# Optimization experiments

Measured on AMD Instinct MI355X. Metric: run time of the kernel, lower is better.

The kernel has to match this reference:

```python
import jax, jax.numpy as jnp
import numpy as np

U, S, D = 4096, 8192, 32
NUM_REGIONS = 128
GA = 0.1


def setup_inputs() -> dict:
    key = jax.random.key(0)
    k1, k2, k3, k4, k5, k6 = jax.random.split(key, 6)
    user_emb = jax.random.normal(k1, (U, D), dtype=jnp.float32) * 0.01
    item_emb = jax.random.normal(k2, (S, D), dtype=jnp.float32) * 0.01
    train_mask = jax.random.randint(k3, (U, S), 0, 2, dtype=jnp.int32)
    true_qos = jax.random.normal(k4, (U, S), dtype=jnp.float32)
    us_lossweight = jax.random.uniform(k5, (U, S), dtype=jnp.float32)
    region_index = jax.random.randint(k6, (U,), 0, NUM_REGIONS, dtype=jnp.int32)
    return {
        "user_emb": user_emb,
        "item_emb": item_emb,
        "train_mask": train_mask,
        "true_qos": true_qos,
        "us_lossweight": us_lossweight,
        "region_index": region_index,
    }


def _region_loss(user_emb, region_index):
    # per-region sums and counts via a single segment reduction
    sums = jax.ops.segment_sum(user_emb, region_index, num_segments=NUM_REGIONS)  # [R, D]
    counts = jax.ops.segment_sum(jnp.ones((user_emb.shape[0],), dtype=user_emb.dtype),
                                 region_index, num_segments=NUM_REGIONS)  # [R]
    cnt = counts[region_index]                      # [U]
    loo_mean = (sums[region_index] - user_emb) / jnp.maximum(cnt - 1.0, 1.0)[:, None]
    dev = jnp.abs(user_emb - loo_mean)              # [U, D]
    # regions with a single user are skipped in the original loop
    valid = (cnt > 1.0)[:, None]
    return jnp.sum(jnp.where(valid, dev, 0.0))


def reference(user_emb, item_emb, train_mask, true_qos, us_lossweight, region_index):
    pre_qos = (user_emb @ item_emb.T) * train_mask.astype(user_emb.dtype)  # [U, S]
    mse = (pre_qos - true_qos) ** 2
    loss = jnp.sum(us_lossweight * mse)
    regionloss = _region_loss(user_emb, region_index)
    return loss + GA * regionloss
```

## Files before the change

kernel.cpp:

```cpp
#include <hip/hip_runtime.h>

#define U 4096
#define S 8192
#define D 32
#define NUM_REGIONS 128
#define GA 0.1f

#define TU 32
#define TI 256
#define UG 8
#define THREADS 256
#define LCAP 256


__global__ __launch_bounds__(THREADS) void fused_kernel(
    const float* __restrict__ user_emb,
    const float* __restrict__ item_emb,
    const int* __restrict__ train_mask,
    const float* __restrict__ true_qos,
    const float* __restrict__ us_lossweight,
    const int* __restrict__ region_index,
    float* __restrict__ loss_accum,
    float* __restrict__ rl_accum) {
    __shared__ float uemb[TU][D];
    __shared__ int   ulist[LCAP];
    __shared__ int   ucnt;
    __shared__ float part[8][D];
    __shared__ float redsum[D];
    __shared__ float wp[THREADS / 64];

    const int ub = blockIdx.x * TU;
    const int sb = blockIdx.y * TI;

    {
        const float4* src = (const float4*)(user_emb + (size_t)ub * D);
        ((float4*)&uemb[0][0])[threadIdx.x] = src[threadIdx.x];
    }
    __syncthreads();

    const int s0 = sb + threadIdx.x;
    const float4* ip = (const float4*)(item_emb + (size_t)s0 * D);

    float acc = 0.0f;
    #pragma unroll 1
    for (int g = 0; g < TU; g += UG) {
        int   m[UG]; float q[UG], w[UG];
        #pragma unroll
        for (int j = 0; j < UG; j++) {
            const size_t b = (size_t)(ub + g + j) * S + s0;
            m[j] = train_mask[b];
            q[j] = true_qos[b];
            w[j] = us_lossweight[b];
        }

        float dsum[UG];
        #pragma unroll
        for (int j = 0; j < UG; j++) dsum[j] = 0.0f;

        #pragma unroll
        for (int k = 0; k < 8; k++) {
            float4 iv = ip[k];
            #pragma unroll
            for (int j = 0; j < UG; j++) {
                float4 uv = *(const float4*)&uemb[g + j][k * 4];
                dsum[j] += uv.x * iv.x + uv.y * iv.y + uv.z * iv.z + uv.w * iv.w;
            }
        }

        #pragma unroll
        for (int j = 0; j < UG; j++) {
            float p = dsum[j] * (float)m[j];
            float e = p - q[j];
            acc += w[j] * e * e;
        }
    }

    #pragma unroll
    for (int off = 32; off > 0; off >>= 1) acc += __shfl_down(acc, off, 64);
    {
        int lane = threadIdx.x & 63, wid = threadIdx.x >> 6;
        if (lane == 0) wp[wid] = acc;
        __syncthreads();
        if (threadIdx.x == 0) {
            float t = 0.0f;
            #pragma unroll
            for (int i = 0; i < THREADS / 64; i++) t += wp[i];
            atomicAdd(loss_accum, t);
        }
    }

    if (blockIdx.y != 0) return;
    const int r = blockIdx.x;

    __syncthreads();
    if (threadIdx.x == 0) ucnt = 0;
    __syncthreads();

    for (int u = threadIdx.x; u < U; u += 256) {
        if (region_index[u] == r) {
            int p = atomicAdd(&ucnt, 1);
            if (p < LCAP) ulist[p] = u;
        }
    }
    __syncthreads();

    const int n = min(ucnt, LCAP);
    const int d = threadIdx.x & (D - 1);
    const int w8 = threadIdx.x >> 5;

    float psum = 0.0f;
    for (int i = w8; i < n; i += 8)
        psum += user_emb[ulist[i] * D + d];
    part[w8][d] = psum;
    __syncthreads();
    if (w8 == 0) {
        float sum = 0.0f;
        #pragma unroll
        for (int i = 0; i < 8; i++) sum += part[i][d];
        redsum[d] = sum;
    }
    __syncthreads();

    float racc = 0.0f;
    if (n > 1) {
        const float inv = 1.0f / (float)(n - 1);
        const float sd = redsum[d];
        for (int i = w8; i < n; i += 8) {
            float e = user_emb[ulist[i] * D + d];
            racc += fabsf(e - (sd - e) * inv);
        }
    }

    #pragma unroll
    for (int off = 32; off > 0; off >>= 1) racc += __shfl_down(racc, off, 64);
    {
        int lane = threadIdx.x & 63, wid = threadIdx.x >> 6;
        if (lane == 0) wp[wid] = racc;
        __syncthreads();
        if (threadIdx.x == 0) {
            float t = 0.0f;
            #pragma unroll
            for (int i = 0; i < THREADS / 64; i++) t += wp[i];
            atomicAdd(rl_accum, t);
        }
    }
}

__global__ void finalize_kernel(const float* __restrict__ loss_acc,
                                const float* __restrict__ rl_acc,
                                float* __restrict__ out) {
    out[0] = loss_acc[0] + GA * rl_acc[0];
}

extern "C" void kernel_launch(void* const* d_in, const int* in_sizes, int n_in,
                              void* d_out, int out_size, void* d_ws, size_t ws_size,
                              hipStream_t stream) {
    const float* user_emb      = (const float*)d_in[0];
    const float* item_emb      = (const float*)d_in[1];
    const int*   train_mask    = (const int*)d_in[2];
    const float* true_qos      = (const float*)d_in[3];
    const float* us_lossweight = (const float*)d_in[4];
    const int*   region_index  = (const int*)d_in[5];
    float* out = (float*)d_out;

    float* ws       = (float*)d_ws;
    float* loss_acc = ws;
    float* rl_acc   = ws + 1;
    hipMemsetAsync(d_ws, 0, 2 * sizeof(float), stream);

    dim3 grid(U / TU, S / TI);
    fused_kernel<<<grid, THREADS, 0, stream>>>(
        user_emb, item_emb, train_mask, true_qos, us_lossweight, region_index,
        loss_acc, rl_acc);

    finalize_kernel<<<1, 1, 0, stream>>>(loss_acc, rl_acc, out);
}
```

Baseline: 375.4 us.

## Compute user-item dot products with split-bf16 MFMA and vectorized loss loads

Replaces the scalar FMA dot-product loop with MFMA 16x16x32 bf16 instructions, splitting each fp32 value into a bf16 high part and a bf16 residual and using three MFMAs to keep roughly fp32 accuracy. The tiling changes to 16 users by 1024 items per block, and each wave covers 256 items in 16-item steps. Mask, qos and weight are read as int4/float4 in the MFMA output layout, and the shared-memory staging of user rows is dropped. The kernel is bound by the 3x128MB stream over the mask, qos and weight arrays, so the main gain expected is wider loads and less ALU work. The cost is extra split arithmetic and a small precision change from dropping the lo*lo term.

After: 377.7 us. No clear change (+0.6%).

```diff
diff --git a/kernel.cpp b/kernel.cpp
--- a/kernel.cpp
+++ b/kernel.cpp
@@ -6,11 +6,28 @@
 #define NUM_REGIONS 128
 #define GA 0.1f
 
-#define TU 32
-#define TI 256
-#define UG 8
+#define WU 16
+#define WI 1024
 #define THREADS 256
 #define LCAP 256
+
+typedef short          frag8_t __attribute__((ext_vector_type(8)));
+typedef unsigned short u16x8_t __attribute__((ext_vector_type(8)));
+typedef float          fx4_t   __attribute__((ext_vector_type(4)));
+
+__device__ inline void split8(const float4 a, const float4 b, frag8_t& hi, frag8_t& lo) {
+    u16x8_t h, l;
+    float vv[8] = {a.x, a.y, a.z, a.w, b.x, b.y, b.z, b.w};
+    #pragma unroll
+    for (int j = 0; j < 8; j++) {
+        unsigned bits = __float_as_uint(vv[j]);
+        h[j] = (unsigned short)(bits >> 16);
+        float r = vv[j] - __uint_as_float(bits & 0xFFFF0000u);
+        l[j] = (unsigned short)(__float_as_uint(r) >> 16);
+    }
+    hi = __builtin_bit_cast(frag8_t, h);
+    lo = __builtin_bit_cast(frag8_t, l);
+}
 
 
 __global__ __launch_bounds__(THREADS) void fused_kernel(
@@ -22,74 +39,62 @@
     const int* __restrict__ region_index,
     float* __restrict__ loss_accum,
     float* __restrict__ rl_accum) {
-    __shared__ float uemb[TU][D];
+    __shared__ float wp[THREADS / 64];
     __shared__ int   ulist[LCAP];
     __shared__ int   ucnt;
     __shared__ float part[8][D];
     __shared__ float redsum[D];
-    __shared__ float wp[THREADS / 64];
 
-    const int ub = blockIdx.x * TU;
-    const int sb = blockIdx.y * TI;
+    const int lane = threadIdx.x & 63;
+    const int wid  = threadIdx.x >> 6;
+    const int n16  = lane & 15;
+    const int g    = lane >> 4;
+    const int kb   = g * 8;
 
+    const int ub      = blockIdx.x * WU;
+    const int it_base = blockIdx.y * WI + wid * 256;
+
+    frag8_t uh, ul;
     {
-        const float4* src = (const float4*)(user_emb + (size_t)ub * D);
-        ((float4*)&uemb[0][0])[threadIdx.x] = src[threadIdx.x];
+        const float* up = user_emb + (ub + n16) * D + kb;
+        split8(*(const float4*)up, *(const float4*)(up + 4), uh, ul);
     }
-    __syncthreads();
 
-    const int s0 = sb + threadIdx.x;
-    const float4* ip = (const float4*)(item_emb + (size_t)s0 * D);
+    const unsigned soff = (unsigned)(ub + n16) * S + it_base + g * 4;
+    const int*   mp  = train_mask    + soff;
+    const float* qp  = true_qos      + soff;
+    const float* wtp = us_lossweight + soff;
+    const float* ip  = item_emb + (it_base + n16) * D + kb;
 
     float acc = 0.0f;
-    #pragma unroll 1
-    for (int g = 0; g < TU; g += UG) {
-        int   m[UG]; float q[UG], w[UG];
-        #pragma unroll
-        for (int j = 0; j < UG; j++) {
-            const size_t b = (size_t)(ub + g + j) * S + s0;
-            m[j] = train_mask[b];
-            q[j] = true_qos[b];
-            w[j] = us_lossweight[b];
-        }
+    for (int t = 0; t < 16; t++) {
+        int4   m4 = *(const int4*)(mp + t * 16);
+        float4 q4 = *(const float4*)(qp + t * 16);
+        float4 w4 = *(const float4*)(wtp + t * 16);
 
-        float dsum[UG];
-        #pragma unroll
-        for (int j = 0; j < UG; j++) dsum[j] = 0.0f;
+        frag8_t ih, il;
+        split8(*(const float4*)(ip + t * 16 * D),
+               *(const float4*)(ip + t * 16 * D + 4), ih, il);
 
-        #pragma unroll
-        for (int k = 0; k < 8; k++) {
-            float4 iv = ip[k];
-            #pragma unroll
-            for (int j = 0; j < UG; j++) {
-                float4 uv = *(const float4*)&uemb[g + j][k * 4];
-                dsum[j] += uv.x * iv.x + uv.y * iv.y + uv.z * iv.z + uv.w * iv.w;
-            }
-        }
+        fx4_t c = {0.0f, 0.0f, 0.0f, 0.0f};
+        c = __builtin_amdgcn_mfma_f32_16x16x32_bf16(ih, uh, c, 0, 0, 0);
+        c = __builtin_amdgcn_mfma_f32_16x16x32_bf16(il, uh, c, 0, 0, 0);
+        c = __builtin_amdgcn_mfma_f32_16x16x32_bf16(ih, ul, c, 0, 0, 0);
 
-        #pragma unroll
-        for (int j = 0; j < UG; j++) {
-            float p = dsum[j] * (float)m[j];
-            float e = p - q[j];
-            acc += w[j] * e * e;
-        }
+        float p0 = c[0] * (float)m4.x; float e0 = p0 - q4.x; acc += w4.x * e0 * e0;
+        float p1 = c[1] * (float)m4.y; float e1 = p1 - q4.y; acc += w4.y * e1 * e1;
+        float p2 = c[2] * (float)m4.z; float e2 = p2 - q4.z; acc += w4.z * e2 * e2;
+        float p3 = c[3] * (float)m4.w; float e3 = p3 - q4.w; acc += w4.w * e3 * e3;
     }
 
     #pragma unroll
     for (int off = 32; off > 0; off >>= 1) acc += __shfl_down(acc, off, 64);
-    {
-        int lane = threadIdx.x & 63, wid = threadIdx.x >> 6;
-        if (lane == 0) wp[wid] = acc;
-        __syncthreads();
-        if (threadIdx.x == 0) {
-            float t = 0.0f;
-            #pragma unroll
-            for (int i = 0; i < THREADS / 64; i++) t += wp[i];
-            atomicAdd(loss_accum, t);
-        }
-    }
+    if (lane == 0) wp[wid] = acc;
+    __syncthreads();
+    if (threadIdx.x == 0)
+        atomicAdd(loss_accum, wp[0] + wp[1] + wp[2] + wp[3]);
 
-    if (blockIdx.y != 0) return;
+    if (blockIdx.y != 0 || blockIdx.x >= NUM_REGIONS) return;
     const int r = blockIdx.x;
 
     __syncthreads();
@@ -133,17 +138,10 @@
 
     #pragma unroll
     for (int off = 32; off > 0; off >>= 1) racc += __shfl_down(racc, off, 64);
-    {
-        int lane = threadIdx.x & 63, wid = threadIdx.x >> 6;
-        if (lane == 0) wp[wid] = racc;
-        __syncthreads();
-        if (threadIdx.x == 0) {
-            float t = 0.0f;
-            #pragma unroll
-            for (int i = 0; i < THREADS / 64; i++) t += wp[i];
-            atomicAdd(rl_accum, t);
-        }
-    }
+    if (lane == 0) wp[wid] = racc;
+    __syncthreads();
+    if (threadIdx.x == 0)
+        atomicAdd(rl_accum, wp[0] + wp[1] + wp[2] + wp[3]);
 }
 
 __global__ void finalize_kernel(const float* __restrict__ loss_acc,
@@ -168,7 +166,7 @@
     float* rl_acc   = ws + 1;
     hipMemsetAsync(d_ws, 0, 2 * sizeof(float), stream);
 
-    dim3 grid(U / TU, S / TI);
+    dim3 grid(U / WU, S / WI);
     fused_kernel<<<grid, THREADS, 0, stream>>>(
         user_emb, item_emb, train_mask, true_qos, us_lossweight, region_index,
         loss_acc, rl_acc);
```
